# Performance work log

Measured on AMD Instinct MI355X. Metric: run time of the kernel, lower is better.

The kernel has to match this reference:

```python
import jax, jax.numpy as jnp
import numpy as np

N, E, D_IN, D_HID, D_OUT = 100000, 1600000, 128, 128, 40

def _sage_pool(x, src, dst, Wp, bp, Ws, Wn, b, n_nodes):
    # DGL SAGEConv 'pool': h_pool = relu(fc_pool(x)); h_neigh = max over in-neighbors;
    # out = fc_self(x) + fc_neigh(h_neigh) + bias
    hp = jax.nn.relu(x @ Wp + bp)                       # [N, d]
    msg = hp[src]                                        # [E, d] gather
    agg = jax.ops.segment_max(msg, dst, num_segments=n_nodes)  # [N, d] scatter-max
    agg = jnp.where(jnp.isfinite(agg), agg, 0.0)         # zero-in-degree nodes -> 0
    return x @ Ws + agg @ Wn + b

def setup_inputs() -> dict:
    key = jax.random.key(0)
    ks = jax.random.split(key, 14)
    def lin(k, i, o):
        return jax.random.normal(k, (i, o), dtype=jnp.float32) / np.sqrt(i)
    return {
        "in_feat": jax.random.normal(ks[0], (N, D_IN), dtype=jnp.float32),
        "src": jax.random.randint(ks[1], (E,), 0, N),
        "dst": jax.random.randint(ks[2], (E,), 0, N),
        "Wp1": lin(ks[3], D_IN, D_IN), "bp1": jnp.zeros((D_IN,), jnp.float32),
        "Ws1": lin(ks[4], D_IN, D_HID), "Wn1": lin(ks[5], D_IN, D_HID),
        "b1": jnp.zeros((D_HID,), jnp.float32),
        "Wp2": lin(ks[6], D_HID, D_HID), "bp2": jnp.zeros((D_HID,), jnp.float32),
        "Ws2": lin(ks[7], D_HID, D_OUT), "Wn2": lin(ks[8], D_HID, D_OUT),
        "b2": jnp.zeros((D_OUT,), jnp.float32),
    }

def reference(in_feat, src, dst, Wp1, bp1, Ws1, Wn1, b1, Wp2, bp2, Ws2, Wn2, b2):
    h = _sage_pool(in_feat, src, dst, Wp1, bp1, Ws1, Wn1, b1, N)
    h = jax.nn.relu(h)
    # dropout is identity at inference (eval mode)
    return _sage_pool(h, src, dst, Wp2, bp2, Ws2, Wn2, b2, N)
```

## Files before the change

kernel.cpp:

```cpp
#include <hip/hip_runtime.h>
#include <stdint.h>

#define NN 100000
#define NE 1600000
#define NBK 391
#define NPOOL 782
#define NPART 782

using u16 = unsigned short;
using u32 = unsigned int;

typedef __attribute__((ext_vector_type(8))) short bf16x8;
typedef __attribute__((ext_vector_type(4))) float f32x4;

__device__ inline u16 f2b(float f){
  u32 u = __float_as_uint(f);
  u32 r = (u + 0x7fffu + ((u >> 16) & 1u)) >> 16;
  return (u16)r;
}

__device__ inline bf16x8 cvt8(const float* __restrict__ p){
  float4 a = *(const float4*)p;
  float4 b = *(const float4*)(p + 4);
  union { u32 w[4]; bf16x8 v; } u;
  u.w[0] = (u32)f2b(a.x) | ((u32)f2b(a.y) << 16);
  u.w[1] = (u32)f2b(a.z) | ((u32)f2b(a.w) << 16);
  u.w[2] = (u32)f2b(b.x) | ((u32)f2b(b.y) << 16);
  u.w[3] = (u32)f2b(b.z) | ((u32)f2b(b.w) << 16);
  return u.v;
}

__global__ __launch_bounds__(512)
void k_prep(const float* __restrict__ Wp1, const float* __restrict__ Ws1,
            const float* __restrict__ Wn1, const float* __restrict__ Wp2,
            const float* __restrict__ Ws2, const float* __restrict__ Wn2,
            u16* __restrict__ wpT1, u16* __restrict__ wc1T,
            u16* __restrict__ wpT2, u16* __restrict__ wc2T,
            const int* __restrict__ dst, int* __restrict__ cb){
  __shared__ int hcb[NBK];
  const int tid = threadIdx.x;
  for (int i = tid; i < NBK; i += 512) hcb[i] = 0;
  __syncthreads();
  int e0 = blockIdx.x * 2048 + tid;
  #pragma unroll
  for (int j = 0; j < 4; j++){
    int e = e0 + j * 512;
    if (e < NE) atomicAdd(&hcb[dst[e] >> 8], 1);
  }
  int i = blockIdx.x * 512 + tid;
  if (i < 16384){ int n = i >> 7, k = i & 127;
    wpT1[n*128 + k] = f2b(Wp1[k*128 + n]);
    wpT2[n*128 + k] = f2b(Wp2[k*128 + n]);
  }
  if (i < 32768){ int n = i >> 8, k = i & 255;
    float v = (k < 128) ? Ws1[k*128 + n] : Wn1[(k-128)*128 + n];
    wc1T[n*256 + k] = f2b(v);
  }
  if (i < 12288){ int n = i >> 8, k = i & 255;
    float v = 0.f;
    if (n < 40) v = (k < 128) ? Ws2[k*40 + n] : Wn2[(k-128)*40 + n];
    wc2T[n*256 + k] = f2b(v);
  }
  __syncthreads();
  for (int i2 = tid; i2 < NBK; i2 += 512)
    if (hcb[i2]) atomicAdd(&cb[i2], hcb[i2]);
}

__global__ __launch_bounds__(512)
void k_pp(const float* __restrict__ x, const u16* __restrict__ wpT1,
          const float* __restrict__ bp1, u16* __restrict__ hp,
          const int* __restrict__ src, const int* __restrict__ dst,
          const int* __restrict__ cb, int* __restrict__ curB,
          u32* __restrict__ part){
  __shared__ __align__(16) char smem[34816];
  const int tid = threadIdx.x;
  if (blockIdx.x < NPOOL){
    u16* W_lds = (u16*)smem;
    const int row0 = blockIdx.x * 128;
    const int wave = tid >> 6, lane = tid & 63;
    const int colb = lane & 15;
    const int koff = (lane >> 4) * 8;
    for (int c = tid; c < 128 * 16; c += 512){
      int n = c >> 4, kc = c & 15;
      *(uint4*)&W_lds[n * 136 + kc * 8] = *(const uint4*)&wpT1[n * 128 + kc * 8];
    }
    __syncthreads();
    const int rA = min(row0 + wave * 16 + colb, NN - 1);
    f32x4 acc[8] = {};
    #pragma unroll
    for (int k0 = 0; k0 < 128; k0 += 64){
      bf16x8 af0 = cvt8(&x[(size_t)rA * 128 + k0 + koff]);
      bf16x8 af1 = cvt8(&x[(size_t)rA * 128 + k0 + 32 + koff]);
      #pragma unroll
      for (int nt = 0; nt < 8; nt++){
        const u16* Wr = &W_lds[(nt * 16 + colb) * 136 + k0];
        bf16x8 b0 = *(const bf16x8*)&Wr[koff];
        bf16x8 b1 = *(const bf16x8*)&Wr[32 + koff];
        acc[nt] = __builtin_amdgcn_mfma_f32_16x16x32_bf16(af0, b0, acc[nt], 0, 0, 0);
        acc[nt] = __builtin_amdgcn_mfma_f32_16x16x32_bf16(af1, b1, acc[nt], 0, 0, 0);
      }
    }
    const int rowc = wave * 16 + ((lane >> 4) << 2);
    #pragma unroll
    for (int nt = 0; nt < 8; nt++){
      int col = nt * 16 + colb;
      float bv = bp1[col];
      #pragma unroll
      for (int r = 0; r < 4; r++){
        int gr = row0 + rowc + r;
        if (gr < NN)
          hp[(size_t)gr * 128 + col] = f2b(fmaxf(acc[nt][r] + bv, 0.f));
      }
    }
  } else {
    int* hist = (int*)smem;
    int* scn  = hist + NBK;
    int* cur  = scn  + NBK;
    int* base = cur  + NBK;
    int2* stage = (int2*)(base + NBK);
    int* s512 = (int*)stage;
    const int e0 = (blockIdx.x - NPOOL) * 2048;
    const int cnt = min(2048, NE - e0);
    for (int i = tid; i < NBK; i += 512) hist[i] = 0;
    __syncthreads();
    int2 ed[4];
    #pragma unroll
    for (int j = 0; j < 4; j++){
      int e = e0 + j * 512 + tid;
      if (e < NE){
        ed[j].x = src[e]; ed[j].y = dst[e];
        atomicAdd(&hist[ed[j].y >> 8], 1);
      }
    }
    __syncthreads();
    int cv = (tid < NBK) ? cb[tid] : 0;
    s512[tid] = cv;
    __syncthreads();
    #pragma unroll
    for (int off = 1; off < 512; off <<= 1){
      int t = (tid >= off) ? s512[tid - off] : 0;
      __syncthreads();
      s512[tid] += t;
      __syncthreads();
    }
    int gex = s512[tid] - cv;
    int hv = (tid < NBK) ? hist[tid] : 0;
    if (tid < NBK) base[tid] = gex + (hv ? atomicAdd(&curB[tid], hv) : 0);
    __syncthreads();
    s512[tid] = hv;
    __syncthreads();
    #pragma unroll
    for (int off = 1; off < 512; off <<= 1){
      int t = (tid >= off) ? s512[tid - off] : 0;
      __syncthreads();
      s512[tid] += t;
      __syncthreads();
    }
    if (tid < NBK){ int ex = s512[tid] - hv; scn[tid] = ex; cur[tid] = ex; }
    __syncthreads();
    #pragma unroll
    for (int j = 0; j < 4; j++){
      int e = e0 + j * 512 + tid;
      if (e < NE){
        int slot = atomicAdd(&cur[ed[j].y >> 8], 1);
        stage[slot] = ed[j];
      }
    }
    __syncthreads();
    for (int i = tid; i < cnt; i += 512){
      int2 p = stage[i];
      int b = p.y >> 8;
      part[base[b] + (i - scn[b])] = ((u32)(p.y & 255) << 17) | (u32)p.x;
    }
  }
}

__global__ __launch_bounds__(512) void k_bsort(const u32* __restrict__ part,
                                               const int* __restrict__ cb,
                                               int* __restrict__ rp,
                                               int* __restrict__ esrc){
  __shared__ int s512[512];
  __shared__ int cnt[256], sc[256], cur[256];
  __shared__ int lohi[2];
  const int tid = threadIdx.x;
  const int b = blockIdx.x;
  int cv = (tid < NBK) ? cb[tid] : 0;
  s512[tid] = cv;
  __syncthreads();
  #pragma unroll
  for (int off = 1; off < 512; off <<= 1){
    int t = (tid >= off) ? s512[tid - off] : 0;
    __syncthreads();
    s512[tid] += t;
    __syncthreads();
  }
  if (tid == b){ lohi[0] = s512[tid] - cv; lohi[1] = s512[tid]; }
  if (tid < 256) cnt[tid] = 0;
  __syncthreads();
  const int lo = lohi[0], hi = lohi[1];
  for (int i = lo + tid; i < hi; i += 512)
    atomicAdd(&cnt[part[i] >> 17], 1);
  __syncthreads();
  if (tid < 256) sc[tid] = cnt[tid];
  __syncthreads();
  #pragma unroll
  for (int off = 1; off < 256; off <<= 1){
    int t = (tid < 256 && tid >= off) ? sc[tid - off] : 0;
    __syncthreads();
    if (tid < 256) sc[tid] += t;
    __syncthreads();
  }
  if (tid < 256){
    int ex = sc[tid] - cnt[tid];
    int n = (b << 8) + tid;
    if (n < NN) rp[n] = lo + ex;
    cur[tid] = lo + ex;
  }
  if (b == NBK - 1 && tid == 0) rp[NN] = hi;
  __syncthreads();
  for (int i = lo + tid; i < hi; i += 512){
    u32 p = part[i];
    int pos = atomicAdd(&cur[p >> 17], 1);
    esrc[pos] = (int)(p & 0x1FFFFu);
  }
}

__global__ void k_agg(const u16* __restrict__ hp, const int* __restrict__ rp,
                      const int* __restrict__ esrc, u16* __restrict__ agg){
  int node = blockIdx.x * 4 + (threadIdx.x >> 6);
  if (node >= NN) return;
  const int lane = threadIdx.x & 63;
  const int half = lane >> 5;
  const int l32  = lane & 31;
  const int lo = rp[node], hi = rp[node + 1];
  u32 m0 = 0, m1 = 0;
  for (int i = lo; i < hi; i += 16){
    int s[8];
    #pragma unroll
    for (int j = 0; j < 8; j++){
      int ii = i + 2 * j + half; if (ii >= hi) ii = hi - 1;
      s[j] = esrc[ii];
    }
    uint2 v[8];
    #pragma unroll
    for (int j = 0; j < 8; j++)
      v[j] = *(const uint2*)&hp[(size_t)s[j] * 128 + l32 * 4];
    #pragma unroll
    for (int j = 0; j < 8; j++){
      asm("v_pk_max_u16 %0, %0, %1" : "+v"(m0) : "v"(v[j].x));
      asm("v_pk_max_u16 %0, %0, %1" : "+v"(m1) : "v"(v[j].y));
    }
  }
  u32 t0 = (u32)__shfl_xor((int)m0, 32);
  u32 t1 = (u32)__shfl_xor((int)m1, 32);
  asm("v_pk_max_u16 %0, %0, %1" : "+v"(m0) : "v"(t0));
  asm("v_pk_max_u16 %0, %0, %1" : "+v"(m1) : "v"(t1));
  if (half == 0)
    *(uint2*)&agg[(size_t)node * 128 + l32 * 4] = make_uint2(m0, m1);
}

template<int K, int NOUT, int NOUTR, bool A1F32, bool HASA2, bool RELU, bool OUTF32>
__global__ __launch_bounds__(512)
void k_dgemm(const void* __restrict__ A1p, const u16* __restrict__ A2,
             const u16* __restrict__ Wt, const float* __restrict__ bias,
             void* __restrict__ outp)
{
  constexpr int KP  = K + 8;
  constexpr int NTI = NOUT / 16;
  __shared__ u16 W_lds[NOUT * KP];
  const int tid  = threadIdx.x;
  const int row0 = blockIdx.x * 128;
  const int wave = tid >> 6, lane = tid & 63;
  const int colb = lane & 15;
  const int koff = (lane >> 4) * 8;

  for (int c = tid; c < NOUT * (K / 8); c += 512){
    int n = c / (K / 8), kc = c % (K / 8);
    *(uint4*)&W_lds[n * KP + kc * 8] = *(const uint4*)&Wt[n * K + kc * 8];
  }
  __syncthreads();

  const int rA = min(row0 + wave * 16 + colb, NN - 1);
  f32x4 acc[NTI] = {};

  #pragma unroll
  for (int k0 = 0; k0 < K; k0 += 64){
    bf16x8 af0, af1;
    if (A1F32 && k0 < 128){
      const float* A = (const float*)A1p;
      af0 = cvt8(&A[(size_t)rA * 128 + k0 + koff]);
      af1 = cvt8(&A[(size_t)rA * 128 + k0 + 32 + koff]);
    } else {
      const u16* A = (HASA2 && k0 >= 128) ? A2 : (const u16*)A1p;
      int kb = (HASA2 && k0 >= 128) ? (k0 - 128) : k0;
      af0 = *(const bf16x8*)&A[(size_t)rA * 128 + kb + koff];
      af1 = *(const bf16x8*)&A[(size_t)rA * 128 + kb + 32 + koff];
    }
    #pragma unroll
    for (int nt = 0; nt < NTI; nt++){
      const u16* Wr = &W_lds[(nt * 16 + colb) * KP + k0];
      bf16x8 b0 = *(const bf16x8*)&Wr[koff];
      bf16x8 b1 = *(const bf16x8*)&Wr[32 + koff];
      acc[nt] = __builtin_amdgcn_mfma_f32_16x16x32_bf16(af0, b0, acc[nt], 0, 0, 0);
      acc[nt] = __builtin_amdgcn_mfma_f32_16x16x32_bf16(af1, b1, acc[nt], 0, 0, 0);
    }
  }

  const int rowc = wave * 16 + ((lane >> 4) << 2);
  #pragma unroll
  for (int nt = 0; nt < NTI; nt++){
    int col = nt * 16 + colb;
    if (col >= NOUTR) continue;
    float bv = bias[col];
    #pragma unroll
    for (int r = 0; r < 4; r++){
      int gr = row0 + rowc + r;
      if (gr >= NN) continue;
      float v = acc[nt][r] + bv;
      if (RELU) v = fmaxf(v, 0.f);
      if (OUTF32) ((float*)outp)[(size_t)gr * NOUTR + col] = v;
      else        ((u16*)outp)[(size_t)gr * NOUTR + col] = f2b(v);
    }
  }
}

extern "C" void kernel_launch(void* const* d_in, const int* in_sizes, int n_in,
                              void* d_out, int out_size, void* d_ws, size_t ws_size,
                              hipStream_t stream){
  const float* x   = (const float*)d_in[0];
  const int*   src = (const int*)d_in[1];
  const int*   dst = (const int*)d_in[2];
  const float* Wp1 = (const float*)d_in[3];
  const float* bp1 = (const float*)d_in[4];
  const float* Ws1 = (const float*)d_in[5];
  const float* Wn1 = (const float*)d_in[6];
  const float* b1  = (const float*)d_in[7];
  const float* Wp2 = (const float*)d_in[8];
  const float* bp2 = (const float*)d_in[9];
  const float* Ws2 = (const float*)d_in[10];
  const float* Wn2 = (const float*)d_in[11];
  const float* b2  = (const float*)d_in[12];

  char* ws = (char*)d_ws;
  u16* wpT1 = (u16*)(ws + 0);
  u16* wc1T = (u16*)(ws + 32768);
  u16* wpT2 = (u16*)(ws + 98304);
  u16* wc2T = (u16*)(ws + 131072);
  int* cb   = (int*)(ws + 155648);
  int* curB = (int*)(ws + 157696);
  int* rp   = (int*)(ws + 161792);
  u32* part = (u32*)(ws + 561920);
  u16* h    = (u16*)(ws + 561920);
  int* esrc = (int*)(ws + 26161920);
  u16* hp   = (u16*)(ws + 32561920);
  u16* agg  = (u16*)(ws + 58161920);

  hipMemsetAsync(ws + 155648, 0, 4096, stream);
  k_prep<<<(NE + 2047) / 2048, 512, 0, stream>>>(Wp1, Ws1, Wn1, Wp2, Ws2, Wn2,
                                                 wpT1, wc1T, wpT2, wc2T, dst, cb);
  k_pp<<<NPOOL + NPART, 512, 0, stream>>>(x, wpT1, bp1, hp, src, dst, cb, curB, part);
  k_bsort<<<NBK, 512, 0, stream>>>(part, cb, rp, esrc);

  k_agg<<<(NN + 3) / 4, 256, 0, stream>>>(hp, rp, esrc, agg);
  k_dgemm<256,128,128, true ,true ,true ,false>
      <<<(NN + 127) / 128, 512, 0, stream>>>(x, agg, wc1T, b1, h);
  k_dgemm<128,128,128, false,false,true ,false>
      <<<(NN + 127) / 128, 512, 0, stream>>>(h, nullptr, wpT2, bp2, hp);
  k_agg<<<(NN + 3) / 4, 256, 0, stream>>>(hp, rp, esrc, agg);
  k_dgemm<256, 48, 40, false,true ,false,true >
      <<<(NN + 127) / 128, 512, 0, stream>>>(h, agg, wc2T, b2, d_out);
}
```

Baseline: 244.0 us.

## Fuse neighbor max-aggregation into the combine GEMM kernel

Replaces the separate aggregation kernel and combine GEMM with one kernel. Each wave gathers and max-reduces 16 nodes' neighbor features into an LDS band, then runs MFMA directly against it, with weights read from global memory instead of staged in LDS. This removes the agg write and re-read and one launch per layer. In exchange, gather parallelism drops from 4 nodes per 256-thread block to 16 nodes serially per wave, and weights are fetched per wave from global/cache.

```diff
diff --git a/kernel.cpp b/kernel.cpp
--- a/kernel.cpp
+++ b/kernel.cpp
@@ -225,38 +225,102 @@
   }
 }
 
-__global__ void k_agg(const u16* __restrict__ hp, const int* __restrict__ rp,
-                      const int* __restrict__ esrc, u16* __restrict__ agg){
-  int node = blockIdx.x * 4 + (threadIdx.x >> 6);
-  if (node >= NN) return;
-  const int lane = threadIdx.x & 63;
-  const int half = lane >> 5;
-  const int l32  = lane & 31;
-  const int lo = rp[node], hi = rp[node + 1];
-  u32 m0 = 0, m1 = 0;
-  for (int i = lo; i < hi; i += 16){
-    int s[8];
-    #pragma unroll
-    for (int j = 0; j < 8; j++){
-      int ii = i + 2 * j + half; if (ii >= hi) ii = hi - 1;
-      s[j] = esrc[ii];
-    }
-    uint2 v[8];
-    #pragma unroll
-    for (int j = 0; j < 8; j++)
-      v[j] = *(const uint2*)&hp[(size_t)s[j] * 128 + l32 * 4];
-    #pragma unroll
-    for (int j = 0; j < 8; j++){
-      asm("v_pk_max_u16 %0, %0, %1" : "+v"(m0) : "v"(v[j].x));
-      asm("v_pk_max_u16 %0, %0, %1" : "+v"(m1) : "v"(v[j].y));
-    }
-  }
-  u32 t0 = (u32)__shfl_xor((int)m0, 32);
-  u32 t1 = (u32)__shfl_xor((int)m1, 32);
-  asm("v_pk_max_u16 %0, %0, %1" : "+v"(m0) : "v"(t0));
-  asm("v_pk_max_u16 %0, %0, %1" : "+v"(m1) : "v"(t1));
-  if (half == 0)
-    *(uint2*)&agg[(size_t)node * 128 + l32 * 4] = make_uint2(m0, m1);
+template<int NOUT, int NOUTR, bool A1F32, bool RELU, bool OUTF32>
+__global__ __launch_bounds__(512)
+void k_fcat(const void* __restrict__ A1p, const u16* __restrict__ hp,
+            const int* __restrict__ rp, const int* __restrict__ esrc,
+            const u16* __restrict__ Wt, const float* __restrict__ bias,
+            void* __restrict__ outp)
+{
+  constexpr int KPB = 136;
+  constexpr int NTI = NOUT / 16;
+  __shared__ u16 G_lds[8 * 16 * KPB];
+  const int tid  = threadIdx.x;
+  const int row0 = blockIdx.x * 128;
+  const int wave = tid >> 6, lane = tid & 63;
+  const int half = lane >> 5, l32 = lane & 31;
+  const int colb = lane & 15;
+  const int koff = (lane >> 4) * 8;
+  u16* band = &G_lds[wave * 16 * KPB];
+
+  for (int j = 0; j < 16; j++){
+    int node = row0 + wave * 16 + j;
+    u32 m0 = 0, m1 = 0;
+    if (node < NN){
+      int lo = rp[node], hi = rp[node + 1];
+      for (int i = lo; i < hi; i += 16){
+        int s[8];
+        #pragma unroll
+        for (int t = 0; t < 8; t++){
+          int ii = i + 2 * t + half; if (ii >= hi) ii = hi - 1;
+          s[t] = esrc[ii];
+        }
+        uint2 v[8];
+        #pragma unroll
+        for (int t = 0; t < 8; t++)
+          v[t] = *(const uint2*)&hp[(size_t)s[t] * 128 + l32 * 4];
+        #pragma unroll
+        for (int t = 0; t < 8; t++){
+          asm("v_pk_max_u16 %0, %0, %1" : "+v"(m0) : "v"(v[t].x));
+          asm("v_pk_max_u16 %0, %0, %1" : "+v"(m1) : "v"(v[t].y));
+        }
+      }
+    }
+    u32 t0 = (u32)__shfl_xor((int)m0, 32);
+    u32 t1 = (u32)__shfl_xor((int)m1, 32);
+    asm("v_pk_max_u16 %0, %0, %1" : "+v"(m0) : "v"(t0));
+    asm("v_pk_max_u16 %0, %0, %1" : "+v"(m1) : "v"(t1));
+    if (half == 0)
+      *(uint2*)&band[j * KPB + l32 * 4] = make_uint2(m0, m1);
+  }
+
+  const u16* Gr = &band[colb * KPB];
+  const int rA = min(row0 + wave * 16 + colb, NN - 1);
+  f32x4 acc[NTI] = {};
+
+  #pragma unroll
+  for (int k0 = 0; k0 < 256; k0 += 64){
+    bf16x8 af0, af1;
+    if (k0 < 128){
+      if (A1F32){
+        const float* A = (const float*)A1p;
+        af0 = cvt8(&A[(size_t)rA * 128 + k0 + koff]);
+        af1 = cvt8(&A[(size_t)rA * 128 + k0 + 32 + koff]);
+      } else {
+        const u16* A = (const u16*)A1p;
+        af0 = *(const bf16x8*)&A[(size_t)rA * 128 + k0 + koff];
+        af1 = *(const bf16x8*)&A[(size_t)rA * 128 + k0 + 32 + koff];
+      }
+    } else {
+      af0 = *(const bf16x8*)&Gr[(k0 - 128) + koff];
+      af1 = *(const bf16x8*)&Gr[(k0 - 128) + 32 + koff];
+    }
+    #pragma unroll
+    for (int nt = 0; nt < NTI; nt++){
+      const u16* Wr = &Wt[(nt * 16 + colb) * 256 + k0];
+      bf16x8 b0 = *(const bf16x8*)&Wr[koff];
+      bf16x8 b1 = *(const bf16x8*)&Wr[32 + koff];
+      acc[nt] = __builtin_amdgcn_mfma_f32_16x16x32_bf16(af0, b0, acc[nt], 0, 0, 0);
+      acc[nt] = __builtin_amdgcn_mfma_f32_16x16x32_bf16(af1, b1, acc[nt], 0, 0, 0);
+    }
+  }
+
+  const int rowc = wave * 16 + ((lane >> 4) << 2);
+  #pragma unroll
+  for (int nt = 0; nt < NTI; nt++){
+    int col = nt * 16 + colb;
+    if (col >= NOUTR) continue;
+    float bv = bias[col];
+    #pragma unroll
+    for (int r = 0; r < 4; r++){
+      int gr = row0 + rowc + r;
+      if (gr >= NN) continue;
+      float v = acc[nt][r] + bv;
+      if (RELU) v = fmaxf(v, 0.f);
+      if (OUTF32) ((float*)outp)[(size_t)gr * NOUTR + col] = v;
+      else        ((u16*)outp)[(size_t)gr * NOUTR + col] = f2b(v);
+    }
+  }
 }
 
 template<int K, int NOUT, int NOUTR, bool A1F32, bool HASA2, bool RELU, bool OUTF32>
@@ -353,7 +417,6 @@
   u16* h    = (u16*)(ws + 561920);
   int* esrc = (int*)(ws + 26161920);
   u16* hp   = (u16*)(ws + 32561920);
-  u16* agg  = (u16*)(ws + 58161920);
 
   hipMemsetAsync(ws + 155648, 0, 4096, stream);
   k_prep<<<(NE + 2047) / 2048, 512, 0, stream>>>(Wp1, Ws1, Wn1, Wp2, Ws2, Wn2,
@@ -361,12 +424,10 @@
   k_pp<<<NPOOL + NPART, 512, 0, stream>>>(x, wpT1, bp1, hp, src, dst, cb, curB, part);
   k_bsort<<<NBK, 512, 0, stream>>>(part, cb, rp, esrc);
 
-  k_agg<<<(NN + 3) / 4, 256, 0, stream>>>(hp, rp, esrc, agg);
-  k_dgemm<256,128,128, true ,true ,true ,false>
-      <<<(NN + 127) / 128, 512, 0, stream>>>(x, agg, wc1T, b1, h);
+  k_fcat<128,128, true ,true ,false>
+      <<<(NN + 127) / 128, 512, 0, stream>>>(x, hp, rp, esrc, wc1T, b1, h);
   k_dgemm<128,128,128, false,false,true ,false>
       <<<(NN + 127) / 128, 512, 0, stream>>>(h, nullptr, wpT2, bp2, hp);
-  k_agg<<<(NN + 3) / 4, 256, 0, stream>>>(hp, rp, esrc, agg);
-  k_dgemm<256, 48, 40, false,true ,false,true >
-      <<<(NN + 127) / 128, 512, 0, stream>>>(h, agg, wc2T, b2, d_out);
-}
+  k_fcat< 48, 40, false,false,true >
+      <<<(NN + 127) / 128, 512, 0, stream>>>(h, hp, rp, esrc, wc2T, b2, d_out);
+}
```

Measured after the change: 319.2 us. 1.31x slower.
